# Kernel optimization log

Measured on AMD Instinct MI355X. Metric: run time of the kernel, lower is better.

## Reference

```python
import jax, jax.numpy as jnp
import numpy as np

B, S, D, H = 2, 2048, 1024, 16
DH = D // H


def setup_inputs() -> dict:
    key = jax.random.key(0)
    ks = jax.random.split(key, 6)
    scale = 1.0 / np.sqrt(D)
    x = jax.random.normal(ks[0], (B, S, D), dtype=jnp.float32)
    mask = jnp.tril(jnp.ones((S, S), dtype=jnp.int32))  # causal 0/1 mask
    Wq = jax.random.normal(ks[1], (D, D), dtype=jnp.float32) * scale
    Wk = jax.random.normal(ks[2], (D, D), dtype=jnp.float32) * scale
    Wv = jax.random.normal(ks[3], (D, D), dtype=jnp.float32) * scale
    Wo = jax.random.normal(ks[4], (D, D), dtype=jnp.float32) * scale
    z = jnp.zeros((D,), dtype=jnp.float32)
    return {"x": x, "mask": mask, "Wq": Wq, "bq": z, "Wk": Wk, "bk": z,
            "Wv": Wv, "bv": z, "Wo": Wo, "bo": z}


def reference(x, mask, Wq, bq, Wk, bk, Wv, bv, Wo, bo):
    # Linear projections (torch Linear: x @ W.T + b; here W stored as [in, out])
    Q = x @ Wq + bq
    K = x @ Wk + bk
    V = x @ Wv + bv
    # [B, S, D] -> [B, H, S, DH]
    Q = Q.reshape(B, S, H, DH).transpose(0, 2, 1, 3)
    K = K.reshape(B, S, H, DH).transpose(0, 2, 1, 3)
    V = V.reshape(B, S, H, DH).transpose(0, 2, 1, 3)
    # scores: [B, H, S, S]
    attn = jnp.einsum('bhqd,bhkd->bhqk', Q, K) / jnp.sqrt(jnp.float32(DH))
    attn = jnp.where(mask == 0, jnp.float32(-1e9), attn)
    scores = jax.nn.softmax(attn, axis=-1)
    # dropout is identity in eval mode
    out = jnp.einsum('bhqk,bhkd->bhqd', scores, V)
    out = out.transpose(0, 2, 1, 3).reshape(B, S, D)
    return out @ Wo + bo
```

## Files before the change

kernel.cpp:

```cpp
#include <hip/hip_runtime.h>
#include <hip/hip_bf16.h>


typedef short bf16x8 __attribute__((ext_vector_type(8)));
typedef float f32x4  __attribute__((ext_vector_type(4)));
typedef short s16x4  __attribute__((ext_vector_type(4)));

#define BB 2
#define SS 2048
#define DD 1024
#define HH 16
#define DHH 64

__device__ __forceinline__ unsigned short f2bf(float f) {
    unsigned u = __builtin_bit_cast(unsigned, f);
    u += 0x7FFFu + ((u >> 16) & 1u);
    return (unsigned short)(u >> 16);
}
__device__ __forceinline__ void cp16(const unsigned short* g, unsigned short* l) {
    __builtin_amdgcn_global_load_lds(
        (const __attribute__((address_space(1))) unsigned int*)(g),
        (__attribute__((address_space(3))) unsigned int*)(l), 16, 0, 0);
}

__global__ __launch_bounds__(256) void cvt_bf16(
    const float* __restrict__ src, unsigned short* __restrict__ dst, int n) {
    int i = (blockIdx.x * 256 + threadIdx.x) * 4;
    if (i >= n) return;
    float4 v = *reinterpret_cast<const float4*>(src + i);
    s16x4 p;
    p[0] = (short)f2bf(v.x); p[1] = (short)f2bf(v.y);
    p[2] = (short)f2bf(v.z); p[3] = (short)f2bf(v.w);
    *reinterpret_cast<s16x4*>(dst + i) = p;
}

__global__ __launch_bounds__(256) void transpose_w(
    const float* __restrict__ w0, const float* __restrict__ w1,
    const float* __restrict__ w2, const float* __restrict__ w3,
    unsigned short* __restrict__ dst) {
    __shared__ float tile[64][65];
    const float* src = blockIdx.z == 0 ? w0 : blockIdx.z == 1 ? w1
                     : blockIdx.z == 2 ? w2 : w3;
    unsigned short* out = dst + (size_t)blockIdx.z * (DD * DD);
    int bx = blockIdx.x * 64, by = blockIdx.y * 64;
    int tx = threadIdx.x, ty = threadIdx.y;
    #pragma unroll
    for (int i = 0; i < 64; i += 4)
        tile[ty + i][tx] = src[(size_t)(by + ty + i) * DD + bx + tx];
    __syncthreads();
    #pragma unroll
    for (int i = 0; i < 64; i += 4)
        out[(size_t)(bx + ty + i) * DD + by + tx] = f2bf(tile[tx][ty + i]);
}

__global__ __launch_bounds__(256) void gemm_qkv(
    const unsigned short* __restrict__ A, const unsigned short* __restrict__ Wt,
    const float* __restrict__ b0, const float* __restrict__ b1,
    const float* __restrict__ b2,
    unsigned short* __restrict__ d0, unsigned short* __restrict__ d1,
    unsigned short* __restrict__ d2) {
    __shared__ __align__(16) unsigned short As[128 * 64];
    __shared__ __align__(16) unsigned short Bs[128 * 64];

    const int tid  = threadIdx.x;
    const int lane = tid & 63;
    const int w    = tid >> 6;
    const int col  = lane & 15;
    const int quad = lane >> 4;
    const int wm   = (w >> 1) * 64;
    const int wn   = (w & 1) * 64;
    const int mb   = blockIdx.y * 128;
    const int nb   = blockIdx.x * 128;

    const int r8 = lane >> 3, gg = lane & 7;
    const int srcoff = ((gg ^ r8) * 8);
    const int cswz = col & 7;

    f32x4 acc[4][4];
    #pragma unroll
    for (int i = 0; i < 4; i++)
        #pragma unroll
        for (int j = 0; j < 4; j++) acc[i][j] = (f32x4){0.f, 0.f, 0.f, 0.f};

    for (int kt = 0; kt < 1024; kt += 64) {
        __syncthreads();
        #pragma unroll
        for (int it = 0; it < 4; it++) {
            int row = w * 32 + it * 8 + r8;
            cp16(A  + (size_t)(mb + row) * 1024 + kt + srcoff, As + (w * 32 + it * 8) * 64);
            cp16(Wt + (size_t)(nb + row) * 1024 + kt + srcoff, Bs + (w * 32 + it * 8) * 64);
        }
        __syncthreads();
        #pragma unroll
        for (int kk = 0; kk < 64; kk += 32) {
            const int kg = (kk >> 3) + quad;
            const int pos = ((kg ^ cswz) * 8);
            bf16x8 af[4], bfr[4];
            #pragma unroll
            for (int i = 0; i < 4; i++)
                af[i] = *reinterpret_cast<const bf16x8*>(As + (wm + i * 16 + col) * 64 + pos);
            #pragma unroll
            for (int j = 0; j < 4; j++)
                bfr[j] = *reinterpret_cast<const bf16x8*>(Bs + (wn + j * 16 + col) * 64 + pos);
            #pragma unroll
            for (int i = 0; i < 4; i++)
                #pragma unroll
                for (int j = 0; j < 4; j++)
                    acc[i][j] = __builtin_amdgcn_mfma_f32_16x16x32_bf16(af[i], bfr[j], acc[i][j], 0, 0, 0);
        }
    }

    const float QSCALE = 0.125f * 1.44269504f;
    #pragma unroll
    for (int i = 0; i < 4; i++) {
        int mg = mb + wm + i * 16 + quad * 4;
        #pragma unroll
        for (int j = 0; j < 4; j++) {
            int ng = nb + wn + j * 16 + col;
            int sel = ng >> 10, n2 = ng & 1023;
            int h = n2 >> 6, dd2 = n2 & 63;
            int b = mg >> 11, s = mg & 2047;
            int bh = b * HH + h;
            const float* bp = sel == 0 ? b0 : sel == 1 ? b1 : b2;
            float bbv = bp[n2];
            if (sel == 0) {
                #pragma unroll
                for (int r = 0; r < 4; r++)
                    d0[((size_t)bh * SS + s + r) * DHH + dd2] = f2bf((acc[i][j][r] + bbv) * QSCALE);
            } else if (sel == 1) {
                #pragma unroll
                for (int r = 0; r < 4; r++)
                    d1[((size_t)bh * SS + s + r) * DHH + dd2] = f2bf(acc[i][j][r] + bbv);
            } else {
                s16x4 pack;
                #pragma unroll
                for (int r = 0; r < 4; r++) pack[r] = (short)f2bf(acc[i][j][r] + bbv);
                *reinterpret_cast<s16x4*>(d2 + ((size_t)bh * DHH + dd2) * SS + s) = pack;
            }
        }
    }
}

__global__ __launch_bounds__(256) void gemm_out(
    const unsigned short* __restrict__ A, const unsigned short* __restrict__ Wt,
    const float* __restrict__ b0, float* __restrict__ d0f) {
    __shared__ __align__(16) unsigned short As[128 * 64];
    __shared__ __align__(16) unsigned short Bs[64 * 64];

    const int tid  = threadIdx.x;
    const int lane = tid & 63;
    const int w    = tid >> 6;
    const int col  = lane & 15;
    const int quad = lane >> 4;
    const int wm   = (w >> 1) * 64;
    const int wn   = (w & 1) * 32;
    const int mb   = blockIdx.y * 128;
    const int nb   = blockIdx.x * 64;

    const int r8 = lane >> 3, gg = lane & 7;
    const int srcoff = ((gg ^ r8) * 8);
    const int cswz = col & 7;

    f32x4 acc[4][2];
    #pragma unroll
    for (int i = 0; i < 4; i++)
        #pragma unroll
        for (int j = 0; j < 2; j++) acc[i][j] = (f32x4){0.f, 0.f, 0.f, 0.f};

    for (int kt = 0; kt < 1024; kt += 64) {
        __syncthreads();
        #pragma unroll
        for (int it = 0; it < 4; it++) {
            int row = w * 32 + it * 8 + r8;
            cp16(A + (size_t)(mb + row) * 1024 + kt + srcoff, As + (w * 32 + it * 8) * 64);
        }
        {
            int row = w * 16 + (r8 & 7);
            cp16(Wt + (size_t)(nb + w * 16 + r8) * 1024 + kt + srcoff, Bs + (w * 16) * 64);
            cp16(Wt + (size_t)(nb + w * 16 + 8 + r8) * 1024 + kt + srcoff, Bs + (w * 16 + 8) * 64);
            (void)row;
        }
        __syncthreads();
        #pragma unroll
        for (int kk = 0; kk < 64; kk += 32) {
            const int kg = (kk >> 3) + quad;
            const int pos = ((kg ^ cswz) * 8);
            bf16x8 af[4], bfr[2];
            #pragma unroll
            for (int i = 0; i < 4; i++)
                af[i] = *reinterpret_cast<const bf16x8*>(As + (wm + i * 16 + col) * 64 + pos);
            #pragma unroll
            for (int j = 0; j < 2; j++)
                bfr[j] = *reinterpret_cast<const bf16x8*>(Bs + (wn + j * 16 + col) * 64 + pos);
            #pragma unroll
            for (int i = 0; i < 4; i++)
                #pragma unroll
                for (int j = 0; j < 2; j++)
                    acc[i][j] = __builtin_amdgcn_mfma_f32_16x16x32_bf16(af[i], bfr[j], acc[i][j], 0, 0, 0);
        }
    }

    #pragma unroll
    for (int i = 0; i < 4; i++) {
        int mg = mb + wm + i * 16 + quad * 4;
        #pragma unroll
        for (int j = 0; j < 2; j++) {
            int ng = nb + wn + j * 16 + col;
            float bbv = b0[ng];
            #pragma unroll
            for (int r = 0; r < 4; r++)
                d0f[(size_t)(mg + r) * 1024 + ng] = acc[i][j][r] + bbv;
        }
    }
}

__global__ __launch_bounds__(256) void attn(
    const unsigned short* __restrict__ Q, const unsigned short* __restrict__ K,
    const unsigned short* __restrict__ Vt, unsigned short* __restrict__ O) {
    __shared__ __align__(16) unsigned short Ks[64 * 64];
    __shared__ __align__(16) unsigned short Vs[64 * 64];
    __shared__ __align__(16) unsigned short Ps[4][16 * 72];

    const int tid  = threadIdx.x;
    const int lane = tid & 63;
    const int w    = tid >> 6;
    const int col  = lane & 15;
    const int quad = lane >> 4;
    const int bh   = blockIdx.x & 31;
    const int qt   = 31 - (blockIdx.x >> 5);
    const int qb   = qt * 64;
    const int r8 = lane >> 3, gg = lane & 7;
    const int srcoff = ((gg ^ r8) * 8);
    const int cswz = col & 7;

    bf16x8 onesf;
    #pragma unroll
    for (int j = 0; j < 8; j++) onesf[j] = (col == 0) ? (short)0x3F80 : (short)0;

    const int qrow = qb + w * 16 + col;
    const size_t qbase = ((size_t)bh * SS + qrow) * DHH;
    bf16x8 qlo = *reinterpret_cast<const bf16x8*>(Q + qbase + quad * 8);
    bf16x8 qhi = *reinterpret_cast<const bf16x8*>(Q + qbase + 32 + quad * 8);

    f32x4 o[5];
    #pragma unroll
    for (int d = 0; d < 5; d++) o[d] = (f32x4){0.f, 0.f, 0.f, 0.f};
    float m_i[4];
    #pragma unroll
    for (int r = 0; r < 4; r++) m_i[r] = -1e30f;

    for (int kt = 0; kt <= qt; kt++) {
        __syncthreads();
        #pragma unroll
        for (int it = 0; it < 2; it++) {
            int row = w * 16 + it * 8 + r8;
            cp16(K  + ((size_t)bh * SS + kt * 64 + row) * DHH + srcoff,
                 Ks + (w * 16 + it * 8) * 64);
            cp16(Vt + ((size_t)bh * DHH + row) * SS + kt * 64 + srcoff,
                 Vs + (w * 16 + it * 8) * 64);
        }
        __syncthreads();

        f32x4 sc[4];
        #pragma unroll
        for (int nt = 0; nt < 4; nt++) {
            int key = nt * 16 + col;
            bf16x8 klo = *reinterpret_cast<const bf16x8*>(Ks + key * 64 + ((quad       ^ cswz) * 8));
            bf16x8 khi = *reinterpret_cast<const bf16x8*>(Ks + key * 64 + (((4 + quad) ^ cswz) * 8));
            f32x4 z = (f32x4){0.f, 0.f, 0.f, 0.f};
            z = __builtin_amdgcn_mfma_f32_16x16x32_bf16(qlo, klo, z, 0, 0, 0);
            z = __builtin_amdgcn_mfma_f32_16x16x32_bf16(qhi, khi, z, 0, 0, 0);
            sc[nt] = z;
        }
        if (kt == qt) {
            #pragma unroll
            for (int nt = 0; nt < 4; nt++) {
                int kg = kt * 64 + nt * 16 + col;
                #pragma unroll
                for (int r = 0; r < 4; r++) {
                    int qg = qb + w * 16 + quad * 4 + r;
                    if (kg > qg) sc[nt][r] = -3.0e38f;
                }
            }
        }
        float mnew[4];
        bool upd = false;
        #pragma unroll
        for (int r = 0; r < 4; r++) {
            float t = fmaxf(fmaxf(sc[0][r], sc[1][r]), fmaxf(sc[2][r], sc[3][r]));
            t = fmaxf(t, __shfl_xor(t, 1));
            t = fmaxf(t, __shfl_xor(t, 2));
            t = fmaxf(t, __shfl_xor(t, 4));
            t = fmaxf(t, __shfl_xor(t, 8));
            mnew[r] = fmaxf(m_i[r], t);
            upd = upd || (mnew[r] > m_i[r]);
        }
        if (__any(upd)) {
            #pragma unroll
            for (int r = 0; r < 4; r++) {
                float a = exp2f(m_i[r] - mnew[r]);
                #pragma unroll
                for (int d = 0; d < 5; d++) o[d][r] *= a;
            }
        }
        #pragma unroll
        for (int r = 0; r < 4; r++) m_i[r] = mnew[r];

        unsigned short* pw = Ps[w];
        #pragma unroll
        for (int nt = 0; nt < 4; nt++)
            #pragma unroll
            for (int r = 0; r < 4; r++)
                pw[(quad * 4 + r) * 72 + nt * 16 + col] = f2bf(exp2f(sc[nt][r] - mnew[r]));
        bf16x8 pf0 = *reinterpret_cast<const bf16x8*>(pw + col * 72 + quad * 8);
        bf16x8 pf1 = *reinterpret_cast<const bf16x8*>(pw + col * 72 + 32 + quad * 8);
        #pragma unroll
        for (int dt = 0; dt < 4; dt++) {
            int rv = dt * 16 + col;
            bf16x8 vf0 = *reinterpret_cast<const bf16x8*>(Vs + rv * 64 + ((quad       ^ cswz) * 8));
            bf16x8 vf1 = *reinterpret_cast<const bf16x8*>(Vs + rv * 64 + (((4 + quad) ^ cswz) * 8));
            o[dt] = __builtin_amdgcn_mfma_f32_16x16x32_bf16(pf0, vf0, o[dt], 0, 0, 0);
            o[dt] = __builtin_amdgcn_mfma_f32_16x16x32_bf16(pf1, vf1, o[dt], 0, 0, 0);
        }
        o[4] = __builtin_amdgcn_mfma_f32_16x16x32_bf16(pf0, onesf, o[4], 0, 0, 0);
        o[4] = __builtin_amdgcn_mfma_f32_16x16x32_bf16(pf1, onesf, o[4], 0, 0, 0);
    }

    #pragma unroll
    for (int r = 0; r < 4; r++) {
        float lv = __shfl(o[4][r], lane & 48);
        float inv = 1.0f / lv;
        int sq = qb + w * 16 + quad * 4 + r;
        size_t base = ((size_t)(bh >> 4) * SS + sq) * DD + (size_t)(bh & 15) * DHH;
        #pragma unroll
        for (int dt = 0; dt < 4; dt++)
            O[base + dt * 16 + col] = f2bf(o[dt][r] * inv);
    }
}

extern "C" void kernel_launch(void* const* d_in, const int* in_sizes, int n_in,
                              void* d_out, int out_size, void* d_ws, size_t ws_size,
                              hipStream_t stream) {
    (void)in_sizes; (void)n_in; (void)out_size; (void)ws_size;
    const float* x  = (const float*)d_in[0];
    const float* Wq = (const float*)d_in[2];
    const float* bq = (const float*)d_in[3];
    const float* Wk = (const float*)d_in[4];
    const float* bk = (const float*)d_in[5];
    const float* Wv = (const float*)d_in[6];
    const float* bv = (const float*)d_in[7];
    const float* Wo = (const float*)d_in[8];
    const float* bo = (const float*)d_in[9];
    float* out = (float*)d_out;

    char* ws = (char*)d_ws;
    unsigned short* xbf = (unsigned short*)(ws);
    unsigned short* qws = (unsigned short*)(ws + ((size_t)8  << 20));
    unsigned short* kws = (unsigned short*)(ws + ((size_t)16 << 20));
    unsigned short* vws = (unsigned short*)(ws + ((size_t)24 << 20));
    unsigned short* wt  = (unsigned short*)(ws + ((size_t)32 << 20));
    unsigned short* ows = xbf;

    const int nx = BB * SS * DD;
    cvt_bf16<<<dim3(nx / 1024), 256, 0, stream>>>(x, xbf, nx);
    transpose_w<<<dim3(16, 16, 4), dim3(64, 4), 0, stream>>>(Wq, Wk, Wv, Wo, wt);
    gemm_qkv<<<dim3(24, 32), 256, 0, stream>>>(xbf, wt, bq, bk, bv,
                                               qws, kws, vws);
    attn<<<dim3(1024), 256, 0, stream>>>(qws, kws, vws, ows);
    gemm_out<<<dim3(16, 32), 256, 0, stream>>>(ows, wt + (size_t)3 * 1024 * 1024,
                                               bo, out);
}
```

Baseline: 222.2 us.

## Process two key tiles per attention iteration and truncate P to bf16

```diff
diff --git a/kernel.cpp b/kernel.cpp
--- a/kernel.cpp
+++ b/kernel.cpp
@@ -16,6 +16,9 @@
     unsigned u = __builtin_bit_cast(unsigned, f);
     u += 0x7FFFu + ((u >> 16) & 1u);
     return (unsigned short)(u >> 16);
+}
+__device__ __forceinline__ unsigned short f2bf_trunc(float f) {
+    return (unsigned short)(__builtin_bit_cast(unsigned, f) >> 16);
 }
 __device__ __forceinline__ void cp16(const unsigned short* g, unsigned short* l) {
     __builtin_amdgcn_global_load_lds(
@@ -174,12 +177,8 @@
             int row = w * 32 + it * 8 + r8;
             cp16(A + (size_t)(mb + row) * 1024 + kt + srcoff, As + (w * 32 + it * 8) * 64);
         }
-        {
-            int row = w * 16 + (r8 & 7);
-            cp16(Wt + (size_t)(nb + w * 16 + r8) * 1024 + kt + srcoff, Bs + (w * 16) * 64);
-            cp16(Wt + (size_t)(nb + w * 16 + 8 + r8) * 1024 + kt + srcoff, Bs + (w * 16 + 8) * 64);
-            (void)row;
-        }
+        cp16(Wt + (size_t)(nb + w * 16 + r8) * 1024 + kt + srcoff, Bs + (w * 16) * 64);
+        cp16(Wt + (size_t)(nb + w * 16 + 8 + r8) * 1024 + kt + srcoff, Bs + (w * 16 + 8) * 64);
         __syncthreads();
         #pragma unroll
         for (int kk = 0; kk < 64; kk += 32) {
@@ -214,11 +213,11 @@
     }
 }
 
-__global__ __launch_bounds__(256) void attn(
+__global__ __launch_bounds__(256, 3) void attn(
     const unsigned short* __restrict__ Q, const unsigned short* __restrict__ K,
     const unsigned short* __restrict__ Vt, unsigned short* __restrict__ O) {
-    __shared__ __align__(16) unsigned short Ks[64 * 64];
-    __shared__ __align__(16) unsigned short Vs[64 * 64];
+    __shared__ __align__(16) unsigned short Ks[2][64 * 64];
+    __shared__ __align__(16) unsigned short Vs[2][64 * 64];
     __shared__ __align__(16) unsigned short Ps[4][16 * 72];
 
     const int tid  = threadIdx.x;
@@ -232,6 +231,8 @@
     const int r8 = lane >> 3, gg = lane & 7;
     const int srcoff = ((gg ^ r8) * 8);
     const int cswz = col & 7;
+    const int pos0 = (quad       ^ cswz) * 8;
+    const int pos1 = ((4 + quad) ^ cswz) * 8;
 
     bf16x8 onesf;
     #pragma unroll
@@ -249,37 +250,63 @@
     #pragma unroll
     for (int r = 0; r < 4; r++) m_i[r] = -1e30f;
 
-    for (int kt = 0; kt <= qt; kt++) {
+    const int ntiles = qt + 1;
+    for (int t0 = 0; t0 < ntiles; t0 += 2) {
+        const bool two = (t0 + 1 < ntiles);
         __syncthreads();
         #pragma unroll
         for (int it = 0; it < 2; it++) {
             int row = w * 16 + it * 8 + r8;
-            cp16(K  + ((size_t)bh * SS + kt * 64 + row) * DHH + srcoff,
-                 Ks + (w * 16 + it * 8) * 64);
-            cp16(Vt + ((size_t)bh * DHH + row) * SS + kt * 64 + srcoff,
-                 Vs + (w * 16 + it * 8) * 64);
-        }
-        __syncthreads();
-
-        f32x4 sc[4];
+            cp16(K  + ((size_t)bh * SS + t0 * 64 + row) * DHH + srcoff,
+                 Ks[0] + (w * 16 + it * 8) * 64);
+            cp16(Vt + ((size_t)bh * DHH + row) * SS + t0 * 64 + srcoff,
+                 Vs[0] + (w * 16 + it * 8) * 64);
+        }
+        if (two) {
+            #pragma unroll
+            for (int it = 0; it < 2; it++) {
+                int row = w * 16 + it * 8 + r8;
+                cp16(K  + ((size_t)bh * SS + (t0 + 1) * 64 + row) * DHH + srcoff,
+                     Ks[1] + (w * 16 + it * 8) * 64);
+                cp16(Vt + ((size_t)bh * DHH + row) * SS + (t0 + 1) * 64 + srcoff,
+                     Vs[1] + (w * 16 + it * 8) * 64);
+            }
+        }
+        __syncthreads();
+
+        f32x4 sc[8];
         #pragma unroll
         for (int nt = 0; nt < 4; nt++) {
             int key = nt * 16 + col;
-            bf16x8 klo = *reinterpret_cast<const bf16x8*>(Ks + key * 64 + ((quad       ^ cswz) * 8));
-            bf16x8 khi = *reinterpret_cast<const bf16x8*>(Ks + key * 64 + (((4 + quad) ^ cswz) * 8));
+            bf16x8 klo = *reinterpret_cast<const bf16x8*>(Ks[0] + key * 64 + pos0);
+            bf16x8 khi = *reinterpret_cast<const bf16x8*>(Ks[0] + key * 64 + pos1);
             f32x4 z = (f32x4){0.f, 0.f, 0.f, 0.f};
             z = __builtin_amdgcn_mfma_f32_16x16x32_bf16(qlo, klo, z, 0, 0, 0);
             z = __builtin_amdgcn_mfma_f32_16x16x32_bf16(qhi, khi, z, 0, 0, 0);
             sc[nt] = z;
         }
-        if (kt == qt) {
+        if (two) {
             #pragma unroll
             for (int nt = 0; nt < 4; nt++) {
-                int kg = kt * 64 + nt * 16 + col;
+                int key = nt * 16 + col;
+                bf16x8 klo = *reinterpret_cast<const bf16x8*>(Ks[1] + key * 64 + pos0);
+                bf16x8 khi = *reinterpret_cast<const bf16x8*>(Ks[1] + key * 64 + pos1);
+                f32x4 z = (f32x4){0.f, 0.f, 0.f, 0.f};
+                z = __builtin_amdgcn_mfma_f32_16x16x32_bf16(qlo, klo, z, 0, 0, 0);
+                z = __builtin_amdgcn_mfma_f32_16x16x32_bf16(qhi, khi, z, 0, 0, 0);
+                sc[4 + nt] = z;
+            }
+        }
+        if (t0 == qt || (two && t0 + 1 == qt)) {
+            const int sb = (t0 == qt) ? 0 : 4;
+            const int tb = (t0 == qt) ? t0 : t0 + 1;
+            #pragma unroll
+            for (int nt = 0; nt < 4; nt++) {
+                int kg = tb * 64 + nt * 16 + col;
                 #pragma unroll
                 for (int r = 0; r < 4; r++) {
                     int qg = qb + w * 16 + quad * 4 + r;
-                    if (kg > qg) sc[nt][r] = -3.0e38f;
+                    if (kg > qg) sc[sb + nt][r] = -3.0e38f;
                 }
             }
         }
@@ -288,6 +315,8 @@
         #pragma unroll
         for (int r = 0; r < 4; r++) {
             float t = fmaxf(fmaxf(sc[0][r], sc[1][r]), fmaxf(sc[2][r], sc[3][r]));
+            if (two)
+                t = fmaxf(t, fmaxf(fmaxf(sc[4][r], sc[5][r]), fmaxf(sc[6][r], sc[7][r])));
             t = fmaxf(t, __shfl_xor(t, 1));
             t = fmaxf(t, __shfl_xor(t, 2));
             t = fmaxf(t, __shfl_xor(t, 4));
@@ -311,19 +340,40 @@
         for (int nt = 0; nt < 4; nt++)
             #pragma unroll
             for (int r = 0; r < 4; r++)
-                pw[(quad * 4 + r) * 72 + nt * 16 + col] = f2bf(exp2f(sc[nt][r] - mnew[r]));
-        bf16x8 pf0 = *reinterpret_cast<const bf16x8*>(pw + col * 72 + quad * 8);
-        bf16x8 pf1 = *reinterpret_cast<const bf16x8*>(pw + col * 72 + 32 + quad * 8);
-        #pragma unroll
-        for (int dt = 0; dt < 4; dt++) {
-            int rv = dt * 16 + col;
-            bf16x8 vf0 = *reinterpret_cast<const bf16x8*>(Vs + rv * 64 + ((quad       ^ cswz) * 8));
-            bf16x8 vf1 = *reinterpret_cast<const bf16x8*>(Vs + rv * 64 + (((4 + quad) ^ cswz) * 8));
-            o[dt] = __builtin_amdgcn_mfma_f32_16x16x32_bf16(pf0, vf0, o[dt], 0, 0, 0);
-            o[dt] = __builtin_amdgcn_mfma_f32_16x16x32_bf16(pf1, vf1, o[dt], 0, 0, 0);
-        }
-        o[4] = __builtin_amdgcn_mfma_f32_16x16x32_bf16(pf0, onesf, o[4], 0, 0, 0);
-        o[4] = __builtin_amdgcn_mfma_f32_16x16x32_bf16(pf1, onesf, o[4], 0, 0, 0);
+                pw[(quad * 4 + r) * 72 + nt * 16 + col] = f2bf_trunc(exp2f(sc[nt][r] - mnew[r]));
+        {
+            bf16x8 pf0 = *reinterpret_cast<const bf16x8*>(pw + col * 72 + quad * 8);
+            bf16x8 pf1 = *reinterpret_cast<const bf16x8*>(pw + col * 72 + 32 + quad * 8);
+            #pragma unroll
+            for (int dt = 0; dt < 4; dt++) {
+                int rv = dt * 16 + col;
+                bf16x8 vf0 = *reinterpret_cast<const bf16x8*>(Vs[0] + rv * 64 + pos0);
+                bf16x8 vf1 = *reinterpret_cast<const bf16x8*>(Vs[0] + rv * 64 + pos1);
+                o[dt] = __builtin_amdgcn_mfma_f32_16x16x32_bf16(pf0, vf0, o[dt], 0, 0, 0);
+                o[dt] = __builtin_amdgcn_mfma_f32_16x16x32_bf16(pf1, vf1, o[dt], 0, 0, 0);
+            }
+            o[4] = __builtin_amdgcn_mfma_f32_16x16x32_bf16(pf0, onesf, o[4], 0, 0, 0);
+            o[4] = __builtin_amdgcn_mfma_f32_16x16x32_bf16(pf1, onesf, o[4], 0, 0, 0);
+        }
+        if (two) {
+            #pragma unroll
+            for (int nt = 0; nt < 4; nt++)
+                #pragma unroll
+                for (int r = 0; r < 4; r++)
+                    pw[(quad * 4 + r) * 72 + nt * 16 + col] = f2bf_trunc(exp2f(sc[4 + nt][r] - mnew[r]));
+            bf16x8 pf0 = *reinterpret_cast<const bf16x8*>(pw + col * 72 + quad * 8);
+            bf16x8 pf1 = *reinterpret_cast<const bf16x8*>(pw + col * 72 + 32 + quad * 8);
+            #pragma unroll
+            for (int dt = 0; dt < 4; dt++) {
+                int rv = dt * 16 + col;
+                bf16x8 vf0 = *reinterpret_cast<const bf16x8*>(Vs[1] + rv * 64 + pos0);
+                bf16x8 vf1 = *reinterpret_cast<const bf16x8*>(Vs[1] + rv * 64 + pos1);
+                o[dt] = __builtin_amdgcn_mfma_f32_16x16x32_bf16(pf0, vf0, o[dt], 0, 0, 0);
+                o[dt] = __builtin_amdgcn_mfma_f32_16x16x32_bf16(pf1, vf1, o[dt], 0, 0, 0);
+            }
+            o[4] = __builtin_amdgcn_mfma_f32_16x16x32_bf16(pf0, onesf, o[4], 0, 0, 0);
+            o[4] = __builtin_amdgcn_mfma_f32_16x16x32_bf16(pf1, onesf, o[4], 0, 0, 0);
+        }
     }
 
     #pragma unroll
```

Measured after the change: 212.5 us. 1.05x faster.

## Enlarge attention query tile to 128 rows and load two KV tiles per sync

Applied to the files above, without the earlier changes.

```diff
diff --git a/kernel.cpp b/kernel.cpp
--- a/kernel.cpp
+++ b/kernel.cpp
@@ -16,6 +16,9 @@
     unsigned u = __builtin_bit_cast(unsigned, f);
     u += 0x7FFFu + ((u >> 16) & 1u);
     return (unsigned short)(u >> 16);
+}
+__device__ __forceinline__ unsigned short f2bf_trunc(float f) {
+    return (unsigned short)(__builtin_bit_cast(unsigned, f) >> 16);
 }
 __device__ __forceinline__ void cp16(const unsigned short* g, unsigned short* l) {
     __builtin_amdgcn_global_load_lds(
@@ -174,12 +177,8 @@
             int row = w * 32 + it * 8 + r8;
             cp16(A + (size_t)(mb + row) * 1024 + kt + srcoff, As + (w * 32 + it * 8) * 64);
         }
-        {
-            int row = w * 16 + (r8 & 7);
-            cp16(Wt + (size_t)(nb + w * 16 + r8) * 1024 + kt + srcoff, Bs + (w * 16) * 64);
-            cp16(Wt + (size_t)(nb + w * 16 + 8 + r8) * 1024 + kt + srcoff, Bs + (w * 16 + 8) * 64);
-            (void)row;
-        }
+        cp16(Wt + (size_t)(nb + w * 16 + r8) * 1024 + kt + srcoff, Bs + (w * 16) * 64);
+        cp16(Wt + (size_t)(nb + w * 16 + 8 + r8) * 1024 + kt + srcoff, Bs + (w * 16 + 8) * 64);
         __syncthreads();
         #pragma unroll
         for (int kk = 0; kk < 64; kk += 32) {
@@ -217,9 +216,9 @@
 __global__ __launch_bounds__(256) void attn(
     const unsigned short* __restrict__ Q, const unsigned short* __restrict__ K,
     const unsigned short* __restrict__ Vt, unsigned short* __restrict__ O) {
-    __shared__ __align__(16) unsigned short Ks[64 * 64];
-    __shared__ __align__(16) unsigned short Vs[64 * 64];
-    __shared__ __align__(16) unsigned short Ps[4][16 * 72];
+    __shared__ __align__(16) unsigned short Ks[2][64 * 64];
+    __shared__ __align__(16) unsigned short Vs[2][64 * 64];
+    __shared__ __align__(16) unsigned short Ps[4][32 * 72];
 
     const int tid  = threadIdx.x;
     const int lane = tid & 63;
@@ -227,115 +226,164 @@
     const int col  = lane & 15;
     const int quad = lane >> 4;
     const int bh   = blockIdx.x & 31;
-    const int qt   = 31 - (blockIdx.x >> 5);
-    const int qb   = qt * 64;
+    const int qt   = 15 - (blockIdx.x >> 5);
+    const int qb   = qt * 128;
+    const int wq   = qb + w * 32;
     const int r8 = lane >> 3, gg = lane & 7;
     const int srcoff = ((gg ^ r8) * 8);
     const int cswz = col & 7;
+    const int pos0 = (quad       ^ cswz) * 8;
+    const int pos1 = ((4 + quad) ^ cswz) * 8;
 
     bf16x8 onesf;
     #pragma unroll
     for (int j = 0; j < 8; j++) onesf[j] = (col == 0) ? (short)0x3F80 : (short)0;
 
-    const int qrow = qb + w * 16 + col;
-    const size_t qbase = ((size_t)bh * SS + qrow) * DHH;
-    bf16x8 qlo = *reinterpret_cast<const bf16x8*>(Q + qbase + quad * 8);
-    bf16x8 qhi = *reinterpret_cast<const bf16x8*>(Q + qbase + 32 + quad * 8);
-
-    f32x4 o[5];
-    #pragma unroll
-    for (int d = 0; d < 5; d++) o[d] = (f32x4){0.f, 0.f, 0.f, 0.f};
-    float m_i[4];
-    #pragma unroll
-    for (int r = 0; r < 4; r++) m_i[r] = -1e30f;
-
-    for (int kt = 0; kt <= qt; kt++) {
+    const size_t qb0 = ((size_t)bh * SS + wq + col) * DHH;
+    const size_t qb1 = ((size_t)bh * SS + wq + 16 + col) * DHH;
+    bf16x8 qf[2][2];
+    qf[0][0] = *reinterpret_cast<const bf16x8*>(Q + qb0 + quad * 8);
+    qf[0][1] = *reinterpret_cast<const bf16x8*>(Q + qb0 + 32 + quad * 8);
+    qf[1][0] = *reinterpret_cast<const bf16x8*>(Q + qb1 + quad * 8);
+    qf[1][1] = *reinterpret_cast<const bf16x8*>(Q + qb1 + 32 + quad * 8);
+
+    f32x4 o[2][4], l[2];
+    #pragma unroll
+    for (int s = 0; s < 2; s++) {
+        l[s] = (f32x4){0.f, 0.f, 0.f, 0.f};
+        #pragma unroll
+        for (int d = 0; d < 4; d++) o[s][d] = (f32x4){0.f, 0.f, 0.f, 0.f};
+    }
+    float m_i[2][4];
+    #pragma unroll
+    for (int s = 0; s < 2; s++)
+        #pragma unroll
+        for (int r = 0; r < 4; r++) m_i[s][r] = -1e30f;
+
+    const int ntiles = 2 * qt + 2;
+    for (int t0 = 0; t0 < ntiles; t0 += 2) {
         __syncthreads();
         #pragma unroll
         for (int it = 0; it < 2; it++) {
             int row = w * 16 + it * 8 + r8;
-            cp16(K  + ((size_t)bh * SS + kt * 64 + row) * DHH + srcoff,
-                 Ks + (w * 16 + it * 8) * 64);
-            cp16(Vt + ((size_t)bh * DHH + row) * SS + kt * 64 + srcoff,
-                 Vs + (w * 16 + it * 8) * 64);
-        }
-        __syncthreads();
-
-        f32x4 sc[4];
-        #pragma unroll
-        for (int nt = 0; nt < 4; nt++) {
-            int key = nt * 16 + col;
-            bf16x8 klo = *reinterpret_cast<const bf16x8*>(Ks + key * 64 + ((quad       ^ cswz) * 8));
-            bf16x8 khi = *reinterpret_cast<const bf16x8*>(Ks + key * 64 + (((4 + quad) ^ cswz) * 8));
-            f32x4 z = (f32x4){0.f, 0.f, 0.f, 0.f};
-            z = __builtin_amdgcn_mfma_f32_16x16x32_bf16(qlo, klo, z, 0, 0, 0);
-            z = __builtin_amdgcn_mfma_f32_16x16x32_bf16(qhi, khi, z, 0, 0, 0);
-            sc[nt] = z;
-        }
-        if (kt == qt) {
+            cp16(K  + ((size_t)bh * SS + t0 * 64 + row) * DHH + srcoff,
+                 Ks[0] + (w * 16 + it * 8) * 64);
+            cp16(Vt + ((size_t)bh * DHH + row) * SS + t0 * 64 + srcoff,
+                 Vs[0] + (w * 16 + it * 8) * 64);
+            cp16(K  + ((size_t)bh * SS + (t0 + 1) * 64 + row) * DHH + srcoff,
+                 Ks[1] + (w * 16 + it * 8) * 64);
+            cp16(Vt + ((size_t)bh * DHH + row) * SS + (t0 + 1) * 64 + srcoff,
+                 Vs[1] + (w * 16 + it * 8) * 64);
+        }
+        __syncthreads();
+
+        #pragma unroll
+        for (int tt = 0; tt < 2; tt++) {
+            const int ktg = t0 + tt;
+            f32x4 sc[2][4];
             #pragma unroll
             for (int nt = 0; nt < 4; nt++) {
-                int kg = kt * 64 + nt * 16 + col;
+                int key = nt * 16 + col;
+                bf16x8 klo = *reinterpret_cast<const bf16x8*>(Ks[tt] + key * 64 + pos0);
+                bf16x8 khi = *reinterpret_cast<const bf16x8*>(Ks[tt] + key * 64 + pos1);
+                f32x4 z0 = (f32x4){0.f, 0.f, 0.f, 0.f};
+                f32x4 z1 = (f32x4){0.f, 0.f, 0.f, 0.f};
+                z0 = __builtin_amdgcn_mfma_f32_16x16x32_bf16(qf[0][0], klo, z0, 0, 0, 0);
+                z0 = __builtin_amdgcn_mfma_f32_16x16x32_bf16(qf[0][1], khi, z0, 0, 0, 0);
+                z1 = __builtin_amdgcn_mfma_f32_16x16x32_bf16(qf[1][0], klo, z1, 0, 0, 0);
+                z1 = __builtin_amdgcn_mfma_f32_16x16x32_bf16(qf[1][1], khi, z1, 0, 0, 0);
+                sc[0][nt] = z0; sc[1][nt] = z1;
+            }
+            if (ktg >= 2 * qt) {
+                #pragma unroll
+                for (int s = 0; s < 2; s++)
+                    #pragma unroll
+                    for (int nt = 0; nt < 4; nt++) {
+                        int kg = ktg * 64 + nt * 16 + col;
+                        #pragma unroll
+                        for (int r = 0; r < 4; r++) {
+                            int qg = wq + s * 16 + quad * 4 + r;
+                            if (kg > qg) sc[s][nt][r] = -3.0e38f;
+                        }
+                    }
+            }
+            float mnew[2][4];
+            bool upd = false;
+            #pragma unroll
+            for (int s = 0; s < 2; s++)
                 #pragma unroll
                 for (int r = 0; r < 4; r++) {
-                    int qg = qb + w * 16 + quad * 4 + r;
-                    if (kg > qg) sc[nt][r] = -3.0e38f;
+                    float t = fmaxf(fmaxf(sc[s][0][r], sc[s][1][r]),
+                                    fmaxf(sc[s][2][r], sc[s][3][r]));
+                    t = fmaxf(t, __shfl_xor(t, 1));
+                    t = fmaxf(t, __shfl_xor(t, 2));
+                    t = fmaxf(t, __shfl_xor(t, 4));
+                    t = fmaxf(t, __shfl_xor(t, 8));
+                    mnew[s][r] = fmaxf(m_i[s][r], t);
+                    upd = upd || (mnew[s][r] > m_i[s][r]);
                 }
-            }
-        }
-        float mnew[4];
-        bool upd = false;
+            if (__any(upd)) {
+                #pragma unroll
+                for (int s = 0; s < 2; s++)
+                    #pragma unroll
+                    for (int r = 0; r < 4; r++) {
+                        float a = exp2f(m_i[s][r] - mnew[s][r]);
+                        #pragma unroll
+                        for (int d = 0; d < 4; d++) o[s][d][r] *= a;
+                        l[s][r] *= a;
+                    }
+            }
+            #pragma unroll
+            for (int s = 0; s < 2; s++)
+                #pragma unroll
+                for (int r = 0; r < 4; r++) m_i[s][r] = mnew[s][r];
+
+            unsigned short* pw = Ps[w];
+            #pragma unroll
+            for (int s = 0; s < 2; s++)
+                #pragma unroll
+                for (int nt = 0; nt < 4; nt++)
+                    #pragma unroll
+                    for (int r = 0; r < 4; r++)
+                        pw[(s * 16 + quad * 4 + r) * 72 + nt * 16 + col] =
+                            f2bf_trunc(exp2f(sc[s][nt][r] - mnew[s][r]));
+            bf16x8 pf[2][2];
+            #pragma unroll
+            for (int s = 0; s < 2; s++) {
+                pf[s][0] = *reinterpret_cast<const bf16x8*>(pw + (s * 16 + col) * 72 + quad * 8);
+                pf[s][1] = *reinterpret_cast<const bf16x8*>(pw + (s * 16 + col) * 72 + 32 + quad * 8);
+            }
+            #pragma unroll
+            for (int dt = 0; dt < 4; dt++) {
+                int rv = dt * 16 + col;
+                bf16x8 vf0 = *reinterpret_cast<const bf16x8*>(Vs[tt] + rv * 64 + pos0);
+                bf16x8 vf1 = *reinterpret_cast<const bf16x8*>(Vs[tt] + rv * 64 + pos1);
+                #pragma unroll
+                for (int s = 0; s < 2; s++) {
+                    o[s][dt] = __builtin_amdgcn_mfma_f32_16x16x32_bf16(pf[s][0], vf0, o[s][dt], 0, 0, 0);
+                    o[s][dt] = __builtin_amdgcn_mfma_f32_16x16x32_bf16(pf[s][1], vf1, o[s][dt], 0, 0, 0);
+                }
+            }
+            #pragma unroll
+            for (int s = 0; s < 2; s++) {
+                l[s] = __builtin_amdgcn_mfma_f32_16x16x32_bf16(pf[s][0], onesf, l[s], 0, 0, 0);
+                l[s] = __builtin_amdgcn_mfma_f32_16x16x32_bf16(pf[s][1], onesf, l[s], 0, 0, 0);
+            }
+        }
+    }
+
+    #pragma unroll
+    for (int s = 0; s < 2; s++)
         #pragma unroll
         for (int r = 0; r < 4; r++) {
-            float t = fmaxf(fmaxf(sc[0][r], sc[1][r]), fmaxf(sc[2][r], sc[3][r]));
-            t = fmaxf(t, __shfl_xor(t, 1));
-            t = fmaxf(t, __shfl_xor(t, 2));
-            t = fmaxf(t, __shfl_xor(t, 4));
-            t = fmaxf(t, __shfl_xor(t, 8));
-            mnew[r] = fmaxf(m_i[r], t);
-            upd = upd || (mnew[r] > m_i[r]);
-        }
-        if (__any(upd)) {
-            #pragma unroll
-            for (int r = 0; r < 4; r++) {
-                float a = exp2f(m_i[r] - mnew[r]);
-                #pragma unroll
-                for (int d = 0; d < 5; d++) o[d][r] *= a;
-            }
-        }
-        #pragma unroll
-        for (int r = 0; r < 4; r++) m_i[r] = mnew[r];
-
-        unsigned short* pw = Ps[w];
-        #pragma unroll
-        for (int nt = 0; nt < 4; nt++)
-            #pragma unroll
-            for (int r = 0; r < 4; r++)
-                pw[(quad * 4 + r) * 72 + nt * 16 + col] = f2bf(exp2f(sc[nt][r] - mnew[r]));
-        bf16x8 pf0 = *reinterpret_cast<const bf16x8*>(pw + col * 72 + quad * 8);
-        bf16x8 pf1 = *reinterpret_cast<const bf16x8*>(pw + col * 72 + 32 + quad * 8);
-        #pragma unroll
-        for (int dt = 0; dt < 4; dt++) {
-            int rv = dt * 16 + col;
-            bf16x8 vf0 = *reinterpret_cast<const bf16x8*>(Vs + rv * 64 + ((quad       ^ cswz) * 8));
-            bf16x8 vf1 = *reinterpret_cast<const bf16x8*>(Vs + rv * 64 + (((4 + quad) ^ cswz) * 8));
-            o[dt] = __builtin_amdgcn_mfma_f32_16x16x32_bf16(pf0, vf0, o[dt], 0, 0, 0);
-            o[dt] = __builtin_amdgcn_mfma_f32_16x16x32_bf16(pf1, vf1, o[dt], 0, 0, 0);
-        }
-        o[4] = __builtin_amdgcn_mfma_f32_16x16x32_bf16(pf0, onesf, o[4], 0, 0, 0);
-        o[4] = __builtin_amdgcn_mfma_f32_16x16x32_bf16(pf1, onesf, o[4], 0, 0, 0);
-    }
-
-    #pragma unroll
-    for (int r = 0; r < 4; r++) {
-        float lv = __shfl(o[4][r], lane & 48);
-        float inv = 1.0f / lv;
-        int sq = qb + w * 16 + quad * 4 + r;
-        size_t base = ((size_t)(bh >> 4) * SS + sq) * DD + (size_t)(bh & 15) * DHH;
-        #pragma unroll
-        for (int dt = 0; dt < 4; dt++)
-            O[base + dt * 16 + col] = f2bf(o[dt][r] * inv);
-    }
+            float lv = __shfl(l[s][r], lane & 48);
+            float inv = 1.0f / lv;
+            int sq = wq + s * 16 + quad * 4 + r;
+            size_t base = ((size_t)(bh >> 4) * SS + sq) * DD + (size_t)(bh & 15) * DHH;
+            #pragma unroll
+            for (int dt = 0; dt < 4; dt++)
+                O[base + dt * 16 + col] = f2bf(o[s][dt][r] * inv);
+        }
 }
 
 extern "C" void kernel_launch(void* const* d_in, const int* in_sizes, int n_in,
@@ -366,7 +414,7 @@
     transpose_w<<<dim3(16, 16, 4), dim3(64, 4), 0, stream>>>(Wq, Wk, Wv, Wo, wt);
     gemm_qkv<<<dim3(24, 32), 256, 0, stream>>>(xbf, wt, bq, bk, bv,
                                                qws, kws, vws);
-    attn<<<dim3(1024), 256, 0, stream>>>(qws, kws, vws, ows);
+    attn<<<dim3(512), 256, 0, stream>>>(qws, kws, vws, ows);
     gemm_out<<<dim3(16, 32), 256, 0, stream>>>(ows, wt + (size_t)3 * 1024 * 1024,
                                                bo, out);
 }
```

After: 243.1 us. +9.4%, slower.
